# Optimization experiments

Measured on AMD Instinct MI355X. Metric: run time of the kernel, lower is better.

The kernel has to match this reference:

```python
import jax, jax.numpy as jnp
import numpy as np

T = 20000          # document length in tokens
EMBED_DIM = 300    # GloVe 840B.300d
STATE_DIM = 400    # 2 * lstm_dim (bidirectional)
HIDDEN = 150       # Scorer hidden_dim default
MAX_N = 10         # span widths 1..10
G_DIM = 2 * STATE_DIM + EMBED_DIM  # 1100


def _mlp3(x, W1, b1, W2, b2, W3, b3):
    # Scorer: Linear -> ReLU -> Linear -> ReLU -> Linear(->1)
    h = jax.nn.relu(x @ W1 + b1)
    h = jax.nn.relu(h @ W2 + b2)
    return h @ W3 + b3


def _span_features(embeds, states, attn_logits):
    """Vectorized SpanEncoder: for every window of width n in 1..MAX_N,
    softmax the per-token attention logits within the window, attention-pool
    the word embeddings, and concat [state_start, state_end, pooled].
    Returns g of shape [sum_n (T-n+1), G_DIM]."""
    gs = []
    for n in range(1, MAX_N + 1):
        S = T - n + 1  # number of width-n spans
        # [n, S] windowed logits and [n, S, E] windowed embeds via shifted slices
        a = jnp.stack([attn_logits[j:j + S] for j in range(n)], axis=0)
        w = jax.nn.softmax(a, axis=0)  # softmax within each span (dim=0 in torch)
        we = jnp.stack([embeds[j:j + S] for j in range(n)], axis=0)
        pooled = jnp.einsum('ns,nse->se', w, we)  # [S, E]
        g = jnp.concatenate([states[:S], states[n - 1:n - 1 + S], pooled], axis=-1)
        gs.append(g)
    return jnp.concatenate(gs, axis=0)


def setup_inputs() -> dict:
    key = jax.random.key(0)
    ks = jax.random.split(key, 16)
    sc = 0.05
    return {
        'embeds': jax.random.normal(ks[0], (T, EMBED_DIM), jnp.float32),
        'states': jax.random.normal(ks[1], (T, STATE_DIM), jnp.float32),
        'attn_W1': jax.random.normal(ks[2], (STATE_DIM, HIDDEN), jnp.float32) * sc,
        'attn_b1': jnp.zeros((HIDDEN,), jnp.float32),
        'attn_W2': jax.random.normal(ks[3], (HIDDEN, HIDDEN), jnp.float32) * sc,
        'attn_b2': jnp.zeros((HIDDEN,), jnp.float32),
        'attn_W3': jax.random.normal(ks[4], (HIDDEN, 1), jnp.float32) * sc,
        'attn_b3': jnp.zeros((1,), jnp.float32),
        'sc_W1': jax.random.normal(ks[5], (G_DIM, HIDDEN), jnp.float32) * sc,
        'sc_b1': jnp.zeros((HIDDEN,), jnp.float32),
        'sc_W2': jax.random.normal(ks[6], (HIDDEN, HIDDEN), jnp.float32) * sc,
        'sc_b2': jnp.zeros((HIDDEN,), jnp.float32),
        'sc_W3': jax.random.normal(ks[7], (HIDDEN, 1), jnp.float32) * sc,
        'sc_b3': jnp.zeros((1,), jnp.float32),
    }


def reference(embeds, states, attn_W1, attn_b1, attn_W2, attn_b2, attn_W3, attn_b3,
              sc_W1, sc_b1, sc_W2, sc_b2, sc_W3, sc_b3):
    # SpanAttention: per-token scalar attention logit from the BiLSTM state
    attn_logits = _mlp3(states, attn_W1, attn_b1, attn_W2, attn_b2, attn_W3, attn_b3)[:, 0]
    # SpanEncoder: ragged windowed attention pooling + boundary-state concat
    g = _span_features(embeds, states, attn_logits)  # [10T-45, 1100]
    # SpanScorer: MLP score per span
    scores = _mlp3(g, sc_W1, sc_b1, sc_W2, sc_b2, sc_W3, sc_b3)[:, 0]
    return scores
```

## Files before the change

kernel.cpp:

```cpp
#include <hip/hip_runtime.h>
#include <hip/hip_bf16.h>
#include <math.h>

#define T_LEN 20000
#define HID 150
#define STR 168

typedef __attribute__((ext_vector_type(8))) __bf16 bf16x8;
typedef __attribute__((ext_vector_type(4))) float f32x4;

__device__ __forceinline__ short f2bf(float f) {
    unsigned u = __float_as_uint(f);
    u = (u + 0x7fff + ((u >> 16) & 1)) >> 16;
    return (short)u;
}

__device__ __forceinline__ unsigned pk2(float a, float b) {
    __hip_bfloat162 h = __float22bfloat162_rn(make_float2(a, b));
    return *(unsigned*)&h;
}

__device__ __forceinline__ bf16x8 cvt8(float4 a, float4 b) {
    union { unsigned u[4]; bf16x8 v; } r;
    r.u[0] = pk2(a.x, a.y);
    r.u[1] = pk2(a.z, a.w);
    r.u[2] = pk2(b.x, b.y);
    r.u[3] = pk2(b.z, b.w);
    return r.v;
}

__device__ __forceinline__ float2 ubf2(unsigned u) {
    return make_float2(__uint_as_float(u << 16),
                       __uint_as_float(u & 0xffff0000u));
}

__global__ __launch_bounds__(256) void wprep(
    const float* __restrict__ sc_W1, const float* __restrict__ attn_W1,
    const float* __restrict__ attn_W2, const float* __restrict__ sc_W2,
    short* __restrict__ frag)
{
    int t = blockIdx.x * 256 + threadIdx.x;
    if (t >= 302080) return;
    float v = 0.f;
    if (t < 199680) {
        int e = t & 7, g = t >> 3;
        int lane = g & 63, h = g >> 6;
        int ks = h % 13, nt = h / 13;
        int k = ks * 32 + (lane >> 4) * 8 + e;
        int cs = (nt % 10) * 16 + (lane & 15);
        if (k < 400 && cs < HID) {
            if (nt < 10)      v = sc_W1[(long)k * HID + cs];
            else if (nt < 20) v = sc_W1[(long)(400 + k) * HID + cs];
            else              v = attn_W1[(long)k * HID + cs];
        }
    } else if (t < 250880) {
        int r = t - 199680;
        int e = r & 7, g = r >> 3;
        int lane = g & 63, h = g >> 6;
        int ks = h % 10, nt = h / 10;
        int k = ks * 32 + (lane >> 4) * 8 + e;
        int cs = nt * 16 + (lane & 15);
        if (k < 300 && cs < HID) v = sc_W1[(long)(800 + k) * HID + cs];
    } else if (t < 276480) {
        int r = t - 250880;
        int e = r & 7, g = r >> 3;
        int lane = g & 63, h = g >> 6;
        int ks = h % 5, nt = h / 5;
        int k = ks * 32 + (lane >> 4) * 8 + e;
        int cs = nt * 16 + (lane & 15);
        if (k < HID && cs < HID) v = attn_W2[(long)k * HID + cs];
    } else {
        int r = t - 276480;
        int e = r & 7, g = r >> 3;
        int lane = g & 63, h = g >> 6;
        int ks = h % 5, nt = h / 5;
        int k = ks * 32 + (lane >> 4) * 8 + e;
        int cs = nt * 16 + (lane & 15);
        if (k < HID && cs < HID) v = sc_W2[(long)k * HID + cs];
    }
    frag[t] = f2bf(v);
}

__global__ __launch_bounds__(384) void mega(
    const float* __restrict__ states, const float* __restrict__ embeds,
    const short* __restrict__ frag,
    const float* __restrict__ scb1, const float* __restrict__ ab1,
    const float* __restrict__ ab2, const float* __restrict__ aW3,
    const float* __restrict__ ab3,
    const float* __restrict__ b2, const float* __restrict__ W3,
    const float* __restrict__ b3,
    float* __restrict__ out)
{
    __shared__ short AsU[19968];
    __shared__ short Us[32 * STR];
    __shared__ short Vs[48 * STR];
    __shared__ short Ps[48 * STR];
    __shared__ short X1s[48 * STR];
    __shared__ float redl[48][6];
    __shared__ float reds[2][32][2];
    __shared__ float Ls[48], ebuf[48];
    __shared__ float sb1[160], ab1s[160], b2s[160], W3s[160];

    const int tid = threadIdx.x;
    const int w = tid >> 6, lane = tid & 63;
    const int ml = lane & 15, kg = lane >> 4;
    const int s0 = blockIdx.x * 32;

    for (int t = tid; t < 160; t += 384) {
        sb1[t]  = (t < HID) ? scb1[t] : 0.f;
        ab1s[t] = (t < HID) ? ab1[t]  : 0.f;
        b2s[t]  = (t < HID) ? b2[t]   : 0.f;
        W3s[t]  = (t < HID) ? W3[t]   : 0.f;
    }

    for (int idx = tid; idx < 2496; idx += 384) {
        int g = idx / 832, r = idx - g * 832;
        int ks = r >> 6, l2 = r & 63;
        int k = ks * 32 + ((l2 >> 4) << 3);
        int row = s0 + g * 16 + (l2 & 15); if (row > T_LEN - 1) row = T_LEN - 1;
        const float* Ar = states + (long)row * 400;
        float4 a0 = make_float4(0.f, 0.f, 0.f, 0.f), a1 = a0;
        if (k + 4 <= 400) a0 = *(const float4*)&Ar[k];
        if (k + 8 <= 400) a1 = *(const float4*)&Ar[k + 4];
        *(bf16x8*)&AsU[idx * 8] = cvt8(a0, a1);
    }
    __syncthreads();

    {
        f32x4 acc[5][3];
        #pragma unroll
        for (int t = 0; t < 5; ++t)
            #pragma unroll
            for (int g = 0; g < 3; ++g)
                acc[t][g] = (f32x4){0.f, 0.f, 0.f, 0.f};

        const short* fb = frag + lane * 8;
        const int t5 = w * 5;
        bf16x8 bcur[5], bnxt[5];
        #pragma unroll
        for (int t = 0; t < 5; ++t)
            bcur[t] = *(const bf16x8*)&fb[((t5 + t) * 13) << 9];

        #pragma unroll
        for (int ks = 0; ks < 13; ++ks) {
            if (ks < 12) {
                #pragma unroll
                for (int t = 0; t < 5; ++t)
                    bnxt[t] = *(const bf16x8*)&fb[((t5 + t) * 13 + ks + 1) << 9];
            }
            bf16x8 af0 = *(const bf16x8*)&AsU[(ks * 64 + lane) * 8];
            bf16x8 af1 = *(const bf16x8*)&AsU[(832 + ks * 64 + lane) * 8];
            bf16x8 af2_ = *(const bf16x8*)&AsU[(1664 + ks * 64 + lane) * 8];
            #pragma unroll
            for (int t = 0; t < 5; ++t) {
                acc[t][0] = __builtin_amdgcn_mfma_f32_16x16x32_bf16(bcur[t], af0, acc[t][0], 0, 0, 0);
                acc[t][1] = __builtin_amdgcn_mfma_f32_16x16x32_bf16(bcur[t], af1, acc[t][1], 0, 0, 0);
                acc[t][2] = __builtin_amdgcn_mfma_f32_16x16x32_bf16(bcur[t], af2_, acc[t][2], 0, 0, 0);
            }
            #pragma unroll
            for (int t = 0; t < 5; ++t) bcur[t] = bnxt[t];
        }

        #pragma unroll
        for (int t = 0; t < 5; ++t) {
            int nt = t5 + t;
            #pragma unroll
            for (int g = 0; g < 3; ++g) {
                if (w < 2) {
                    if (g < 2) {
                        int col0 = nt * 16 + kg * 4;
                        float v[4];
                        #pragma unroll
                        for (int r = 0; r < 4; ++r) {
                            int c = col0 + r;
                            v[r] = (c < HID) ? acc[t][g][r] + sb1[c] : 0.f;
                        }
                        *(uint2*)&Us[(g * 16 + ml) * STR + col0] =
                            make_uint2(pk2(v[0], v[1]), pk2(v[2], v[3]));
                    }
                } else if (w < 4) {
                    int col0 = (nt - 10) * 16 + kg * 4;
                    float v[4];
                    #pragma unroll
                    for (int r = 0; r < 4; ++r) {
                        int c = col0 + r;
                        v[r] = (c < HID) ? acc[t][g][r] : 0.f;
                    }
                    *(uint2*)&Vs[(g * 16 + ml) * STR + col0] =
                        make_uint2(pk2(v[0], v[1]), pk2(v[2], v[3]));
                } else {
                    int col0 = (nt - 20) * 16 + kg * 4;
                    float v[4];
                    #pragma unroll
                    for (int r = 0; r < 4; ++r) {
                        int c = col0 + r;
                        v[r] = (c < HID) ? fmaxf(acc[t][g][r] + ab1s[c], 0.f) : 0.f;
                    }
                    *(uint2*)&X1s[(g * 16 + ml) * STR + col0] =
                        make_uint2(pk2(v[0], v[1]), pk2(v[2], v[3]));
                }
            }
        }
    }
    __syncthreads();

    for (int idx = tid; idx < 1920; idx += 384) {
        int g = idx / 640, r = idx - g * 640;
        int ks = r >> 6, l2 = r & 63;
        int k = ks * 32 + ((l2 >> 4) << 3);
        int row = s0 + g * 16 + (l2 & 15); if (row > T_LEN - 1) row = T_LEN - 1;
        const float* Er = embeds + (long)row * 300;
        float4 a0 = make_float4(0.f, 0.f, 0.f, 0.f), a1 = a0;
        if (k + 4 <= 300) a0 = *(const float4*)&Er[k];
        if (k + 8 <= 300) a1 = *(const float4*)&Er[k + 4];
        *(bf16x8*)&AsU[idx * 8] = cvt8(a0, a1);
    }
    __syncthreads();

    const int tB = (w < 4) ? 2 * w : (w == 4 ? 8 : 9);
    const int nTP = (w < 4) ? 2 : 1;
    {
        f32x4 accP[2][3];
        #pragma unroll
        for (int t = 0; t < 2; ++t)
            #pragma unroll
            for (int g = 0; g < 3; ++g)
                accP[t][g] = (f32x4){0.f, 0.f, 0.f, 0.f};

        const short* fP = frag + 199680 + lane * 8;
        bf16x8 pcur[2], pnxt[2];
        #pragma unroll
        for (int t = 0; t < 2; ++t)
            if (t < nTP) pcur[t] = *(const bf16x8*)&fP[((tB + t) * 10) << 9];

        #pragma unroll
        for (int ks = 0; ks < 10; ++ks) {
            if (ks < 9) {
                #pragma unroll
                for (int t = 0; t < 2; ++t)
                    if (t < nTP) pnxt[t] = *(const bf16x8*)&fP[((tB + t) * 10 + ks + 1) << 9];
            }
            bf16x8 af0 = *(const bf16x8*)&AsU[(ks * 64 + lane) * 8];
            bf16x8 af1 = *(const bf16x8*)&AsU[(640 + ks * 64 + lane) * 8];
            bf16x8 af2_ = *(const bf16x8*)&AsU[(1280 + ks * 64 + lane) * 8];
            #pragma unroll
            for (int t = 0; t < 2; ++t) {
                if (t < nTP) {
                    accP[t][0] = __builtin_amdgcn_mfma_f32_16x16x32_bf16(pcur[t], af0, accP[t][0], 0, 0, 0);
                    accP[t][1] = __builtin_amdgcn_mfma_f32_16x16x32_bf16(pcur[t], af1, accP[t][1], 0, 0, 0);
                    accP[t][2] = __builtin_amdgcn_mfma_f32_16x16x32_bf16(pcur[t], af2_, accP[t][2], 0, 0, 0);
                }
            }
            #pragma unroll
            for (int t = 0; t < 2; ++t) pcur[t] = pnxt[t];
        }

        #pragma unroll
        for (int t = 0; t < 2; ++t) {
            if (t < nTP) {
                int col0 = (tB + t) * 16 + kg * 4;
                #pragma unroll
                for (int g = 0; g < 3; ++g) {
                    float v[4];
                    #pragma unroll
                    for (int r = 0; r < 4; ++r) {
                        int c = col0 + r;
                        v[r] = (c < HID) ? accP[t][g][r] : 0.f;
                    }
                    *(uint2*)&Ps[(g * 16 + ml) * STR + col0] =
                        make_uint2(pk2(v[0], v[1]), pk2(v[2], v[3]));
                }
            }
        }
    }

    {
        const short* fAt2 = frag + 250880 + lane * 8;
        bf16x8 afx[3][5];
        #pragma unroll
        for (int g = 0; g < 3; ++g)
            #pragma unroll
            for (int ks = 0; ks < 5; ++ks)
                afx[g][ks] = *(const bf16x8*)&X1s[(g * 16 + ml) * STR + ks * 32 + kg * 8];

        float score[3][4];
        #pragma unroll
        for (int g = 0; g < 3; ++g)
            #pragma unroll
            for (int r = 0; r < 4; ++r) score[g][r] = 0.f;

        #pragma unroll
        for (int t = 0; t < 2; ++t) {
            if (t < nTP) {
                int nt = tB + t;
                bf16x8 wb[5];
                #pragma unroll
                for (int ks = 0; ks < 5; ++ks)
                    wb[ks] = *(const bf16x8*)&fAt2[(nt * 5 + ks) << 9];
                f32x4 a2[3];
                a2[0] = (f32x4){0.f, 0.f, 0.f, 0.f};
                a2[1] = (f32x4){0.f, 0.f, 0.f, 0.f};
                a2[2] = (f32x4){0.f, 0.f, 0.f, 0.f};
                #pragma unroll
                for (int g = 0; g < 3; ++g)
                    #pragma unroll
                    for (int ks = 0; ks < 5; ++ks)
                        a2[g] = __builtin_amdgcn_mfma_f32_16x16x32_bf16(afx[g][ks], wb[ks], a2[g], 0, 0, 0);
                int col = nt * 16 + ml;
                float b2v = (col < HID) ? ab2[col] : 0.f;
                float w3v = (col < HID) ? aW3[col] : 0.f;
                #pragma unroll
                for (int g = 0; g < 3; ++g)
                    #pragma unroll
                    for (int r = 0; r < 4; ++r)
                        score[g][r] += fmaxf(a2[g][r] + b2v, 0.f) * w3v;
            }
        }
        #pragma unroll
        for (int g = 0; g < 3; ++g)
            #pragma unroll
            for (int r = 0; r < 4; ++r) {
                score[g][r] += __shfl_xor(score[g][r], 1);
                score[g][r] += __shfl_xor(score[g][r], 2);
                score[g][r] += __shfl_xor(score[g][r], 4);
                score[g][r] += __shfl_xor(score[g][r], 8);
            }
        if (ml == 0) {
            #pragma unroll
            for (int g = 0; g < 3; ++g)
                #pragma unroll
                for (int r = 0; r < 4; ++r)
                    redl[g * 16 + kg * 4 + r][w] = score[g][r];
        }
    }
    __syncthreads();

    if (tid < 48) {
        float Lv = redl[tid][0] + redl[tid][1] + redl[tid][2] +
                   redl[tid][3] + redl[tid][4] + redl[tid][5] + ab3[0];
        Ls[tid] = (tid < 41) ? Lv : -1e30f;
    }
    if (tid < 48) {
        float M = -1e30f;
        for (int t = 0; t < 41; ++t) M = fmaxf(M, Ls[t]);
        ebuf[tid] = (tid < 41) ? expf(Ls[tid] - M) : 0.f;
    }

    float Ur[2][20], accp[2][20], den[2];
    const int u = tid & 127;
    if (w >= 4) {
        #pragma unroll
        for (int z = 0; z < 2; ++z) {
            int uz = u + z * 128;
            int iz = uz >> 3, d0z = 20 * (uz & 7);
            const uint2* U2 = (const uint2*)&Us[iz * STR + d0z];
            #pragma unroll
            for (int c = 0; c < 5; ++c) {
                uint2 uv = U2[c];
                float2 a = ubf2(uv.x), b_ = ubf2(uv.y);
                Ur[z][4 * c + 0] = a.x;  Ur[z][4 * c + 1] = a.y;
                Ur[z][4 * c + 2] = b_.x; Ur[z][4 * c + 3] = b_.y;
            }
            #pragma unroll
            for (int d = 0; d < 20; ++d) accp[z][d] = 0.f;
            den[z] = 0.f;
        }
    }
    __syncthreads();

    short* h1p = AsU;

    auto phase1 = [&](int n, int p) {
        #pragma unroll
        for (int z = 0; z < 2; ++z) {
            int uz = u + z * 128;
            int iz = uz >> 3, d0z = 20 * (uz & 7);
            int l = iz + n - 1;
            float e = ebuf[l];
            den[z] += e;
            const uint2* P2 = (const uint2*)&Ps[l * STR + d0z];
            #pragma unroll
            for (int c = 0; c < 5; ++c) {
                uint2 pv = P2[c];
                float2 a = ubf2(pv.x), b_ = ubf2(pv.y);
                accp[z][4 * c + 0] += e * a.x;  accp[z][4 * c + 1] += e * a.y;
                accp[z][4 * c + 2] += e * b_.x; accp[z][4 * c + 3] += e * b_.y;
            }
            float invd = 1.f / den[z];
            const uint2* V2 = (const uint2*)&Vs[l * STR + d0z];
            #pragma unroll
            for (int c = 0; c < 5; ++c) {
                uint2 vv = V2[c];
                float2 a = ubf2(vv.x), b_ = ubf2(vv.y);
                float x0 = fmaxf(Ur[z][4 * c + 0] + a.x  + accp[z][4 * c + 0] * invd, 0.f);
                float x1 = fmaxf(Ur[z][4 * c + 1] + a.y  + accp[z][4 * c + 1] * invd, 0.f);
                float x2 = fmaxf(Ur[z][4 * c + 2] + b_.x + accp[z][4 * c + 2] * invd, 0.f);
                float x3 = fmaxf(Ur[z][4 * c + 3] + b_.y + accp[z][4 * c + 3] * invd, 0.f);
                *(uint2*)&h1p[p * (32 * STR) + iz * STR + d0z + 4 * c] =
                    make_uint2(pk2(x0, x1), pk2(x2, x3));
            }
        }
    };

    if (w >= 4) phase1(1, 0);
    __syncthreads();

    const int mt = w >> 1;
    const int nt0 = (w & 1) * 5;
    const short* fW2 = frag + 276480;
    const float bb = b3[0];

    for (int n = 1; n <= 10; ++n) {
        const int p = (n - 1) & 1;
        if (w >= 4) {
            if (n < 10) phase1(n + 1, 1 - p);
        } else {
            bf16x8 af[5];
            #pragma unroll
            for (int ks = 0; ks < 5; ++ks)
                af[ks] = *(const bf16x8*)&h1p[p * (32 * STR) + (mt * 16 + ml) * STR + ks * 32 + kg * 8];

            float sc[4] = {0.f, 0.f, 0.f, 0.f};
            #pragma unroll
            for (int j = 0; j < 5; ++j) {
                int nt = nt0 + j;
                f32x4 a2 = {0.f, 0.f, 0.f, 0.f};
                #pragma unroll
                for (int ks = 0; ks < 5; ++ks) {
                    bf16x8 bf = *(const bf16x8*)&fW2[(long)(((nt * 5 + ks) << 6) | lane) << 3];
                    a2 = __builtin_amdgcn_mfma_f32_16x16x32_bf16(af[ks], bf, a2, 0, 0, 0);
                }
                int col = nt * 16 + ml;
                float b2v = b2s[col], w3v = W3s[col];
                #pragma unroll
                for (int r = 0; r < 4; ++r)
                    sc[r] += fmaxf(a2[r] + b2v, 0.f) * w3v;
            }
            #pragma unroll
            for (int r = 0; r < 4; ++r) {
                sc[r] += __shfl_xor(sc[r], 1);
                sc[r] += __shfl_xor(sc[r], 2);
                sc[r] += __shfl_xor(sc[r], 4);
                sc[r] += __shfl_xor(sc[r], 8);
            }
            if (ml == 0) {
                #pragma unroll
                for (int r = 0; r < 4; ++r)
                    reds[p][mt * 16 + kg * 4 + r][w & 1] = sc[r];
            }
        }
        __syncthreads();
        if (tid < 32) {
            int S = T_LEN - n + 1;
            int off = (n - 1) * (T_LEN + 1) - (n - 1) * n / 2;
            int sr = s0 + tid;
            if (sr < S) out[off + sr] = reds[p][tid][0] + reds[p][tid][1] + bb;
        }
    }
}

extern "C" void kernel_launch(void* const* d_in, const int* in_sizes, int n_in,
                              void* d_out, int out_size, void* d_ws, size_t ws_size,
                              hipStream_t stream) {
    const float* embeds  = (const float*)d_in[0];
    const float* states  = (const float*)d_in[1];
    const float* attn_W1 = (const float*)d_in[2];
    const float* attn_b1 = (const float*)d_in[3];
    const float* attn_W2 = (const float*)d_in[4];
    const float* attn_b2 = (const float*)d_in[5];
    const float* attn_W3 = (const float*)d_in[6];
    const float* attn_b3 = (const float*)d_in[7];
    const float* sc_W1   = (const float*)d_in[8];
    const float* sc_b1   = (const float*)d_in[9];
    const float* sc_W2   = (const float*)d_in[10];
    const float* sc_b2   = (const float*)d_in[11];
    const float* sc_W3   = (const float*)d_in[12];
    const float* sc_b3   = (const float*)d_in[13];
    float* out = (float*)d_out;

    short* frag = (short*)d_ws;

    wprep<<<1180, 256, 0, stream>>>(sc_W1, attn_W1, attn_W2, sc_W2, frag);
    mega<<<625, 384, 0, stream>>>(states, embeds, frag, sc_b1, attn_b1,
                                  attn_b2, attn_W3, attn_b3,
                                  sc_b2, sc_W3, sc_b3, out);
}
```

Measured before the change: 230.2 us.

## Raise mega kernel to 512 threads with K-chunked staging and reduced LDS

The fused kernel moves from 6 to 8 waves per block and loads the states and embeds tiles in two K-chunks through a smaller shared staging buffer. The attention-MLP second layer now runs before the embeds projection, so its input buffer can be reused for the projected embeds, and the phase-1 pooling work is spread so each thread handles one span slot instead of two. The aim is lower LDS use and register pressure for more resident waves and better latency hiding. The cost is extra barriers per chunk and a changed LDS stride that may affect bank conflicts.

```diff
diff --git a/kernel.cpp b/kernel.cpp
--- a/kernel.cpp
+++ b/kernel.cpp
@@ -4,7 +4,8 @@
 
 #define T_LEN 20000
 #define HID 150
-#define STR 168
+#define STRU 168
+#define STRPV 176
 
 typedef __attribute__((ext_vector_type(8))) __bf16 bf16x8;
 typedef __attribute__((ext_vector_type(4))) float f32x4;
@@ -81,7 +82,56 @@
     frag[t] = f2bf(v);
 }
 
-__global__ __launch_bounds__(384) void mega(
+template<int KC>
+__device__ __forceinline__ void stage48(const float* __restrict__ src, int K,
+                                        int ks0, int s0, int tid, short* RA)
+{
+    for (int idx = tid; idx < 3 * KC * 64; idx += 512) {
+        int g = idx / (KC * 64), r = idx - g * (KC * 64);
+        int ksl = r >> 6, l2 = r & 63;
+        int k = (ks0 + ksl) * 32 + ((l2 >> 4) << 3);
+        int row = s0 + g * 16 + (l2 & 15); if (row > T_LEN - 1) row = T_LEN - 1;
+        const float* Ar = src + (long)row * K;
+        float4 a0 = make_float4(0.f, 0.f, 0.f, 0.f), a1 = a0;
+        if (k + 4 <= K) a0 = *(const float4*)&Ar[k];
+        if (k + 8 <= K) a1 = *(const float4*)&Ar[k + 4];
+        *(bf16x8*)&RA[idx * 8] = cvt8(a0, a1);
+    }
+}
+
+template<int KC, int NT>
+__device__ __forceinline__ void mm48(const short* __restrict__ fb, const short* RA,
+                                     int lane, int ks0, int t0, int kstot,
+                                     f32x4 (*acc)[3])
+{
+    bf16x8 bcur[NT], bnxt[NT];
+    #pragma unroll
+    for (int t = 0; t < NT; ++t)
+        bcur[t] = *(const bf16x8*)&fb[((t0 + t) * kstot + ks0) << 9];
+    #pragma unroll
+    for (int ksl = 0; ksl < KC; ++ksl) {
+        if (ksl < KC - 1) {
+            #pragma unroll
+            for (int t = 0; t < NT; ++t)
+                bnxt[t] = *(const bf16x8*)&fb[((t0 + t) * kstot + ks0 + ksl + 1) << 9];
+        }
+        bf16x8 af0 = *(const bf16x8*)&RA[((0 * KC + ksl) * 64 + lane) * 8];
+        bf16x8 af1 = *(const bf16x8*)&RA[((1 * KC + ksl) * 64 + lane) * 8];
+        bf16x8 af2 = *(const bf16x8*)&RA[((2 * KC + ksl) * 64 + lane) * 8];
+        #pragma unroll
+        for (int t = 0; t < NT; ++t) {
+            acc[t][0] = __builtin_amdgcn_mfma_f32_16x16x32_bf16(bcur[t], af0, acc[t][0], 0, 0, 0);
+            acc[t][1] = __builtin_amdgcn_mfma_f32_16x16x32_bf16(bcur[t], af1, acc[t][1], 0, 0, 0);
+            acc[t][2] = __builtin_amdgcn_mfma_f32_16x16x32_bf16(bcur[t], af2, acc[t][2], 0, 0, 0);
+        }
+        if (ksl < KC - 1) {
+            #pragma unroll
+            for (int t = 0; t < NT; ++t) bcur[t] = bnxt[t];
+        }
+    }
+}
+
+__global__ __launch_bounds__(512, 4) void mega(
     const float* __restrict__ states, const float* __restrict__ embeds,
     const short* __restrict__ frag,
     const float* __restrict__ scb1, const float* __restrict__ ab1,
@@ -91,12 +141,11 @@
     const float* __restrict__ b3,
     float* __restrict__ out)
 {
-    __shared__ short AsU[19968];
-    __shared__ short Us[32 * STR];
-    __shared__ short Vs[48 * STR];
-    __shared__ short Ps[48 * STR];
-    __shared__ short X1s[48 * STR];
-    __shared__ float redl[48][6];
+    __shared__ short RA[10752];
+    __shared__ short XPs[48 * STRPV];
+    __shared__ short Us[32 * STRU];
+    __shared__ short Vs[48 * STRPV];
+    __shared__ float redl[48][8];
     __shared__ float reds[2][32][2];
     __shared__ float Ls[48], ebuf[48];
     __shared__ float sb1[160], ab1s[160], b2s[160], W3s[160];
@@ -106,119 +155,152 @@
     const int ml = lane & 15, kg = lane >> 4;
     const int s0 = blockIdx.x * 32;
 
-    for (int t = tid; t < 160; t += 384) {
+    for (int t = tid; t < 160; t += 512) {
         sb1[t]  = (t < HID) ? scb1[t] : 0.f;
         ab1s[t] = (t < HID) ? ab1[t]  : 0.f;
         b2s[t]  = (t < HID) ? b2[t]   : 0.f;
         W3s[t]  = (t < HID) ? W3[t]   : 0.f;
     }
 
-    for (int idx = tid; idx < 2496; idx += 384) {
-        int g = idx / 832, r = idx - g * 832;
-        int ks = r >> 6, l2 = r & 63;
-        int k = ks * 32 + ((l2 >> 4) << 3);
-        int row = s0 + g * 16 + (l2 & 15); if (row > T_LEN - 1) row = T_LEN - 1;
-        const float* Ar = states + (long)row * 400;
-        float4 a0 = make_float4(0.f, 0.f, 0.f, 0.f), a1 = a0;
-        if (k + 4 <= 400) a0 = *(const float4*)&Ar[k];
-        if (k + 8 <= 400) a1 = *(const float4*)&Ar[k + 4];
-        *(bf16x8*)&AsU[idx * 8] = cvt8(a0, a1);
-    }
-    __syncthreads();
-
+    const short* fb = frag + lane * 8;
+
+    const int nTA = (w < 6) ? 4 : 3;
+    const int t0A = (w < 6) ? 4 * w : 24 + (w - 6) * 3;
     {
-        f32x4 acc[5][3];
-        #pragma unroll
-        for (int t = 0; t < 5; ++t)
+        f32x4 acc[4][3];
+        #pragma unroll
+        for (int t = 0; t < 4; ++t)
             #pragma unroll
             for (int g = 0; g < 3; ++g)
                 acc[t][g] = (f32x4){0.f, 0.f, 0.f, 0.f};
 
-        const short* fb = frag + lane * 8;
-        const int t5 = w * 5;
-        bf16x8 bcur[5], bnxt[5];
-        #pragma unroll
-        for (int t = 0; t < 5; ++t)
-            bcur[t] = *(const bf16x8*)&fb[((t5 + t) * 13) << 9];
-
-        #pragma unroll
-        for (int ks = 0; ks < 13; ++ks) {
-            if (ks < 12) {
-                #pragma unroll
-                for (int t = 0; t < 5; ++t)
-                    bnxt[t] = *(const bf16x8*)&fb[((t5 + t) * 13 + ks + 1) << 9];
-            }
-            bf16x8 af0 = *(const bf16x8*)&AsU[(ks * 64 + lane) * 8];
-            bf16x8 af1 = *(const bf16x8*)&AsU[(832 + ks * 64 + lane) * 8];
-            bf16x8 af2_ = *(const bf16x8*)&AsU[(1664 + ks * 64 + lane) * 8];
-            #pragma unroll
-            for (int t = 0; t < 5; ++t) {
-                acc[t][0] = __builtin_amdgcn_mfma_f32_16x16x32_bf16(bcur[t], af0, acc[t][0], 0, 0, 0);
-                acc[t][1] = __builtin_amdgcn_mfma_f32_16x16x32_bf16(bcur[t], af1, acc[t][1], 0, 0, 0);
-                acc[t][2] = __builtin_amdgcn_mfma_f32_16x16x32_bf16(bcur[t], af2_, acc[t][2], 0, 0, 0);
-            }
-            #pragma unroll
-            for (int t = 0; t < 5; ++t) bcur[t] = bnxt[t];
-        }
-
-        #pragma unroll
-        for (int t = 0; t < 5; ++t) {
-            int nt = t5 + t;
-            #pragma unroll
-            for (int g = 0; g < 3; ++g) {
-                if (w < 2) {
-                    if (g < 2) {
-                        int col0 = nt * 16 + kg * 4;
+        stage48<7>(states, 400, 0, s0, tid, RA);
+        __syncthreads();
+        if (w < 6) mm48<7, 4>(fb, RA, lane, 0, t0A, 13, acc);
+        else       mm48<7, 3>(fb, RA, lane, 0, t0A, 13, acc);
+        __syncthreads();
+        stage48<6>(states, 400, 7, s0, tid, RA);
+        __syncthreads();
+        if (w < 6) mm48<6, 4>(fb, RA, lane, 7, t0A, 13, acc);
+        else       mm48<6, 3>(fb, RA, lane, 7, t0A, 13, acc);
+
+        #pragma unroll
+        for (int t = 0; t < 4; ++t) {
+            if (t < nTA) {
+                int nt = t0A + t;
+                #pragma unroll
+                for (int g = 0; g < 3; ++g) {
+                    if (nt < 10) {
+                        if (g < 2) {
+                            int col0 = nt * 16 + kg * 4;
+                            float v[4];
+                            #pragma unroll
+                            for (int r = 0; r < 4; ++r) {
+                                int c = col0 + r;
+                                v[r] = (c < HID) ? acc[t][g][r] + sb1[c] : 0.f;
+                            }
+                            *(uint2*)&Us[(g * 16 + ml) * STRU + col0] =
+                                make_uint2(pk2(v[0], v[1]), pk2(v[2], v[3]));
+                        }
+                    } else if (nt < 20) {
+                        int col0 = (nt - 10) * 16 + kg * 4;
                         float v[4];
                         #pragma unroll
                         for (int r = 0; r < 4; ++r) {
                             int c = col0 + r;
-                            v[r] = (c < HID) ? acc[t][g][r] + sb1[c] : 0.f;
+                            v[r] = (c < HID) ? acc[t][g][r] : 0.f;
                         }
-                        *(uint2*)&Us[(g * 16 + ml) * STR + col0] =
+                        *(uint2*)&Vs[(g * 16 + ml) * STRPV + col0] =
+                            make_uint2(pk2(v[0], v[1]), pk2(v[2], v[3]));
+                    } else {
+                        int col0 = (nt - 20) * 16 + kg * 4;
+                        float v[4];
+                        #pragma unroll
+                        for (int r = 0; r < 4; ++r) {
+                            int c = col0 + r;
+                            v[r] = (c < HID) ? fmaxf(acc[t][g][r] + ab1s[c], 0.f) : 0.f;
+                        }
+                        *(uint2*)&XPs[(g * 16 + ml) * STRU + col0] =
                             make_uint2(pk2(v[0], v[1]), pk2(v[2], v[3]));
                     }
-                } else if (w < 4) {
-                    int col0 = (nt - 10) * 16 + kg * 4;
-                    float v[4];
+                }
+            }
+        }
+    }
+    __syncthreads();
+
+    const int nTP = (w < 2) ? 2 : 1;
+    const int tB = (w < 2) ? 2 * w : 2 + w;
+    {
+        const short* fAt2 = frag + 250880 + lane * 8;
+        bf16x8 afx[3][5];
+        #pragma unroll
+        for (int g = 0; g < 3; ++g)
+            #pragma unroll
+            for (int ks = 0; ks < 5; ++ks)
+                afx[g][ks] = *(const bf16x8*)&XPs[(g * 16 + ml) * STRU + ks * 32 + kg * 8];
+
+        float score[3][4];
+        #pragma unroll
+        for (int g = 0; g < 3; ++g)
+            #pragma unroll
+            for (int r = 0; r < 4; ++r) score[g][r] = 0.f;
+
+        #pragma unroll
+        for (int t = 0; t < 2; ++t) {
+            if (t < nTP) {
+                int nt = tB + t;
+                bf16x8 wb[5];
+                #pragma unroll
+                for (int ks = 0; ks < 5; ++ks)
+                    wb[ks] = *(const bf16x8*)&fAt2[(nt * 5 + ks) << 9];
+                f32x4 a2[3];
+                a2[0] = (f32x4){0.f, 0.f, 0.f, 0.f};
+                a2[1] = (f32x4){0.f, 0.f, 0.f, 0.f};
+                a2[2] = (f32x4){0.f, 0.f, 0.f, 0.f};
+                #pragma unroll
+                for (int g = 0; g < 3; ++g)
                     #pragma unroll
-                    for (int r = 0; r < 4; ++r) {
-                        int c = col0 + r;
-                        v[r] = (c < HID) ? acc[t][g][r] : 0.f;
-                    }
-                    *(uint2*)&Vs[(g * 16 + ml) * STR + col0] =
-                        make_uint2(pk2(v[0], v[1]), pk2(v[2], v[3]));
-                } else {
-                    int col0 = (nt - 20) * 16 + kg * 4;
-                    float v[4];
+                    for (int ks = 0; ks < 5; ++ks)
+                        a2[g] = __builtin_amdgcn_mfma_f32_16x16x32_bf16(afx[g][ks], wb[ks], a2[g], 0, 0, 0);
+                int col = nt * 16 + ml;
+                float b2v = (col < HID) ? ab2[col] : 0.f;
+                float w3v = (col < HID) ? aW3[col] : 0.f;
+                #pragma unroll
+                for (int g = 0; g < 3; ++g)
                     #pragma unroll
-                    for (int r = 0; r < 4; ++r) {
-                        int c = col0 + r;
-                        v[r] = (c < HID) ? fmaxf(acc[t][g][r] + ab1s[c], 0.f) : 0.f;
-                    }
-                    *(uint2*)&X1s[(g * 16 + ml) * STR + col0] =
-                        make_uint2(pk2(v[0], v[1]), pk2(v[2], v[3]));
-                }
-            }
+                    for (int r = 0; r < 4; ++r)
+                        score[g][r] += fmaxf(a2[g][r] + b2v, 0.f) * w3v;
+            }
+        }
+        #pragma unroll
+        for (int g = 0; g < 3; ++g)
+            #pragma unroll
+            for (int r = 0; r < 4; ++r) {
+                score[g][r] += __shfl_xor(score[g][r], 1);
+                score[g][r] += __shfl_xor(score[g][r], 2);
+                score[g][r] += __shfl_xor(score[g][r], 4);
+                score[g][r] += __shfl_xor(score[g][r], 8);
+            }
+        if (ml == 0) {
+            #pragma unroll
+            for (int g = 0; g < 3; ++g)
+                #pragma unroll
+                for (int r = 0; r < 4; ++r)
+                    redl[g * 16 + kg * 4 + r][w] = score[g][r];
         }
     }
     __syncthreads();
 
-    for (int idx = tid; idx < 1920; idx += 384) {
-        int g = idx / 640, r = idx - g * 640;
-        int ks = r >> 6, l2 = r & 63;
-        int k = ks * 32 + ((l2 >> 4) << 3);
-        int row = s0 + g * 16 + (l2 & 15); if (row > T_LEN - 1) row = T_LEN - 1;
-        const float* Er = embeds + (long)row * 300;
-        float4 a0 = make_float4(0.f, 0.f, 0.f, 0.f), a1 = a0;
-        if (k + 4 <= 300) a0 = *(const float4*)&Er[k];
-        if (k + 8 <= 300) a1 = *(const float4*)&Er[k + 4];
-        *(bf16x8*)&AsU[idx * 8] = cvt8(a0, a1);
-    }
-    __syncthreads();
-
-    const int tB = (w < 4) ? 2 * w : (w == 4 ? 8 : 9);
-    const int nTP = (w < 4) ? 2 : 1;
+    if (tid < 48) {
+        float Lv = redl[tid][0] + redl[tid][1] + redl[tid][2] + redl[tid][3] +
+                   redl[tid][4] + redl[tid][5] + redl[tid][6] + redl[tid][7] + ab3[0];
+        Ls[tid] = (tid < 41) ? Lv : -1e30f;
+        float M = -1e30f;
+        for (int t = 0; t < 41; ++t) M = fmaxf(M, Ls[t]);
+        ebuf[tid] = (tid < 41) ? expf(Ls[tid] - M) : 0.f;
+    }
+
     {
         f32x4 accP[2][3];
         #pragma unroll
@@ -228,32 +310,15 @@
                 accP[t][g] = (f32x4){0.f, 0.f, 0.f, 0.f};
 
         const short* fP = frag + 199680 + lane * 8;
-        bf16x8 pcur[2], pnxt[2];
-        #pragma unroll
-        for (int t = 0; t < 2; ++t)
-            if (t < nTP) pcur[t] = *(const bf16x8*)&fP[((tB + t) * 10) << 9];
-
-        #pragma unroll
-        for (int ks = 0; ks < 10; ++ks) {
-            if (ks < 9) {
-                #pragma unroll
-                for (int t = 0; t < 2; ++t)
-                    if (t < nTP) pnxt[t] = *(const bf16x8*)&fP[((tB + t) * 10 + ks + 1) << 9];
-            }
-            bf16x8 af0 = *(const bf16x8*)&AsU[(ks * 64 + lane) * 8];
-            bf16x8 af1 = *(const bf16x8*)&AsU[(640 + ks * 64 + lane) * 8];
-            bf16x8 af2_ = *(const bf16x8*)&AsU[(1280 + ks * 64 + lane) * 8];
-            #pragma unroll
-            for (int t = 0; t < 2; ++t) {
-                if (t < nTP) {
-                    accP[t][0] = __builtin_amdgcn_mfma_f32_16x16x32_bf16(pcur[t], af0, accP[t][0], 0, 0, 0);
-                    accP[t][1] = __builtin_amdgcn_mfma_f32_16x16x32_bf16(pcur[t], af1, accP[t][1], 0, 0, 0);
-                    accP[t][2] = __builtin_amdgcn_mfma_f32_16x16x32_bf16(pcur[t], af2_, accP[t][2], 0, 0, 0);
-                }
-            }
-            #pragma unroll
-            for (int t = 0; t < 2; ++t) pcur[t] = pnxt[t];
-        }
+        stage48<5>(embeds, 300, 0, s0, tid, RA);
+        __syncthreads();
+        if (w < 2) mm48<5, 2>(fP, RA, lane, 0, tB, 10, accP);
+        else       mm48<5, 1>(fP, RA, lane, 0, tB, 10, accP);
+        __syncthreads();
+        stage48<5>(embeds, 300, 5, s0, tid, RA);
+        __syncthreads();
+        if (w < 2) mm48<5, 2>(fP, RA, lane, 5, tB, 10, accP);
+        else       mm48<5, 1>(fP, RA, lane, 5, tB, 10, accP);
 
         #pragma unroll
         for (int t = 0; t < 2; ++t) {
@@ -267,138 +332,56 @@
                         int c = col0 + r;
                         v[r] = (c < HID) ? accP[t][g][r] : 0.f;
                     }
-                    *(uint2*)&Ps[(g * 16 + ml) * STR + col0] =
+                    *(uint2*)&XPs[(g * 16 + ml) * STRPV + col0] =
                         make_uint2(pk2(v[0], v[1]), pk2(v[2], v[3]));
                 }
             }
         }
     }
 
-    {
-        const short* fAt2 = frag + 250880 + lane * 8;
-        bf16x8 afx[3][5];
-        #pragma unroll
-        for (int g = 0; g < 3; ++g)
-            #pragma unroll
-            for (int ks = 0; ks < 5; ++ks)
-                afx[g][ks] = *(const bf16x8*)&X1s[(g * 16 + ml) * STR + ks * 32 + kg * 8];
-
-        float score[3][4];
-        #pragma unroll
-        for (int g = 0; g < 3; ++g)
-            #pragma unroll
-            for (int r = 0; r < 4; ++r) score[g][r] = 0.f;
-
-        #pragma unroll
-        for (int t = 0; t < 2; ++t) {
-            if (t < nTP) {
-                int nt = tB + t;
-                bf16x8 wb[5];
-                #pragma unroll
-                for (int ks = 0; ks < 5; ++ks)
-                    wb[ks] = *(const bf16x8*)&fAt2[(nt * 5 + ks) << 9];
-                f32x4 a2[3];
-                a2[0] = (f32x4){0.f, 0.f, 0.f, 0.f};
-                a2[1] = (f32x4){0.f, 0.f, 0.f, 0.f};
-                a2[2] = (f32x4){0.f, 0.f, 0.f, 0.f};
-                #pragma unroll
-                for (int g = 0; g < 3; ++g)
-                    #pragma unroll
-                    for (int ks = 0; ks < 5; ++ks)
-                        a2[g] = __builtin_amdgcn_mfma_f32_16x16x32_bf16(afx[g][ks], wb[ks], a2[g], 0, 0, 0);
-                int col = nt * 16 + ml;
-                float b2v = (col < HID) ? ab2[col] : 0.f;
-                float w3v = (col < HID) ? aW3[col] : 0.f;
-                #pragma unroll
-                for (int g = 0; g < 3; ++g)
-                    #pragma unroll
-                    for (int r = 0; r < 4; ++r)
-                        score[g][r] += fmaxf(a2[g][r] + b2v, 0.f) * w3v;
-            }
-        }
-        #pragma unroll
-        for (int g = 0; g < 3; ++g)
-            #pragma unroll
-            for (int r = 0; r < 4; ++r) {
-                score[g][r] += __shfl_xor(score[g][r], 1);
-                score[g][r] += __shfl_xor(score[g][r], 2);
-                score[g][r] += __shfl_xor(score[g][r], 4);
-                score[g][r] += __shfl_xor(score[g][r], 8);
-            }
-        if (ml == 0) {
-            #pragma unroll
-            for (int g = 0; g < 3; ++g)
-                #pragma unroll
-                for (int r = 0; r < 4; ++r)
-                    redl[g * 16 + kg * 4 + r][w] = score[g][r];
-        }
+    float Ur[20], accp[20], den = 0.f;
+    const int u2 = tid - 256;
+    const int iz = u2 >> 3, q = u2 & 7, d0 = 20 * (u2 & 7);
+    if (w >= 4) {
+        const uint2* U2 = (const uint2*)&Us[iz * STRU + d0];
+        #pragma unroll
+        for (int c = 0; c < 5; ++c) {
+            uint2 uv = U2[c];
+            float2 a = ubf2(uv.x), b_ = ubf2(uv.y);
+            Ur[4 * c + 0] = a.x;  Ur[4 * c + 1] = a.y;
+            Ur[4 * c + 2] = b_.x; Ur[4 * c + 3] = b_.y;
+        }
+        #pragma unroll
+        for (int d = 0; d < 20; ++d) accp[d] = 0.f;
     }
     __syncthreads();
 
-    if (tid < 48) {
-        float Lv = redl[tid][0] + redl[tid][1] + redl[tid][2] +
-                   redl[tid][3] + redl[tid][4] + redl[tid][5] + ab3[0];
-        Ls[tid] = (tid < 41) ? Lv : -1e30f;
-    }
-    if (tid < 48) {
-        float M = -1e30f;
-        for (int t = 0; t < 41; ++t) M = fmaxf(M, Ls[t]);
-        ebuf[tid] = (tid < 41) ? expf(Ls[tid] - M) : 0.f;
-    }
-
-    float Ur[2][20], accp[2][20], den[2];
-    const int u = tid & 127;
-    if (w >= 4) {
-        #pragma unroll
-        for (int z = 0; z < 2; ++z) {
-            int uz = u + z * 128;
-            int iz = uz >> 3, d0z = 20 * (uz & 7);
-            const uint2* U2 = (const uint2*)&Us[iz * STR + d0z];
-            #pragma unroll
-            for (int c = 0; c < 5; ++c) {
-                uint2 uv = U2[c];
-                float2 a = ubf2(uv.x), b_ = ubf2(uv.y);
-                Ur[z][4 * c + 0] = a.x;  Ur[z][4 * c + 1] = a.y;
-                Ur[z][4 * c + 2] = b_.x; Ur[z][4 * c + 3] = b_.y;
-            }
-            #pragma unroll
-            for (int d = 0; d < 20; ++d) accp[z][d] = 0.f;
-            den[z] = 0.f;
-        }
-    }
-    __syncthreads();
-
-    short* h1p = AsU;
+    short* h1p = RA;
 
     auto phase1 = [&](int n, int p) {
-        #pragma unroll
-        for (int z = 0; z < 2; ++z) {
-            int uz = u + z * 128;
-            int iz = uz >> 3, d0z = 20 * (uz & 7);
-            int l = iz + n - 1;
-            float e = ebuf[l];
-            den[z] += e;
-            const uint2* P2 = (const uint2*)&Ps[l * STR + d0z];
-            #pragma unroll
-            for (int c = 0; c < 5; ++c) {
-                uint2 pv = P2[c];
-                float2 a = ubf2(pv.x), b_ = ubf2(pv.y);
-                accp[z][4 * c + 0] += e * a.x;  accp[z][4 * c + 1] += e * a.y;
-                accp[z][4 * c + 2] += e * b_.x; accp[z][4 * c + 3] += e * b_.y;
-            }
-            float invd = 1.f / den[z];
-            const uint2* V2 = (const uint2*)&Vs[l * STR + d0z];
-            #pragma unroll
-            for (int c = 0; c < 5; ++c) {
-                uint2 vv = V2[c];
-                float2 a = ubf2(vv.x), b_ = ubf2(vv.y);
-                float x0 = fmaxf(Ur[z][4 * c + 0] + a.x  + accp[z][4 * c + 0] * invd, 0.f);
-                float x1 = fmaxf(Ur[z][4 * c + 1] + a.y  + accp[z][4 * c + 1] * invd, 0.f);
-                float x2 = fmaxf(Ur[z][4 * c + 2] + b_.x + accp[z][4 * c + 2] * invd, 0.f);
-                float x3 = fmaxf(Ur[z][4 * c + 3] + b_.y + accp[z][4 * c + 3] * invd, 0.f);
-                *(uint2*)&h1p[p * (32 * STR) + iz * STR + d0z + 4 * c] =
-                    make_uint2(pk2(x0, x1), pk2(x2, x3));
-            }
+        int l = iz + n - 1;
+        float e = ebuf[l];
+        den += e;
+        const uint2* P2 = (const uint2*)&XPs[l * STRPV + d0];
+        #pragma unroll
+        for (int c = 0; c < 5; ++c) {
+            uint2 pv = P2[c];
+            float2 a = ubf2(pv.x), b_ = ubf2(pv.y);
+            accp[4 * c + 0] += e * a.x;  accp[4 * c + 1] += e * a.y;
+            accp[4 * c + 2] += e * b_.x; accp[4 * c + 3] += e * b_.y;
+        }
+        float invd = 1.f / den;
+        const uint2* V2 = (const uint2*)&Vs[l * STRPV + d0];
+        #pragma unroll
+        for (int c = 0; c < 5; ++c) {
+            uint2 vv = V2[c];
+            float2 a = ubf2(vv.x), b_ = ubf2(vv.y);
+            float x0 = fmaxf(Ur[4 * c + 0] + a.x  + accp[4 * c + 0] * invd, 0.f);
+            float x1 = fmaxf(Ur[4 * c + 1] + a.y  + accp[4 * c + 1] * invd, 0.f);
+            float x2 = fmaxf(Ur[4 * c + 2] + b_.x + accp[4 * c + 2] * invd, 0.f);
+            float x3 = fmaxf(Ur[4 * c + 3] + b_.y + accp[4 * c + 3] * invd, 0.f);
+            *(uint2*)&h1p[p * (32 * STRU) + iz * STRU + d0 + 4 * c] =
+                make_uint2(pk2(x0, x1), pk2(x2, x3));
         }
     };
 
@@ -418,7 +401,7 @@
             bf16x8 af[5];
             #pragma unroll
             for (int ks = 0; ks < 5; ++ks)
-                af[ks] = *(const bf16x8*)&h1p[p * (32 * STR) + (mt * 16 + ml) * STR + ks * 32 + kg * 8];
+                af[ks] = *(const bf16x8*)&h1p[p * (32 * STRU) + (mt * 16 + ml) * STRU + ks * 32 + kg * 8];
 
             float sc[4] = {0.f, 0.f, 0.f, 0.f};
             #pragma unroll
@@ -481,7 +464,7 @@
     short* frag = (short*)d_ws;
 
     wprep<<<1180, 256, 0, stream>>>(sc_W1, attn_W1, attn_W2, sc_W2, frag);
-    mega<<<625, 384, 0, stream>>>(states, embeds, frag, sc_b1, attn_b1,
+    mega<<<625, 512, 0, stream>>>(states, embeds, frag, sc_b1, attn_b1,
                                   attn_b2, attn_W3, attn_b3,
                                   sc_b2, sc_W3, sc_b3, out);
 }
```

Result: slower. 244.2 us (+6.1%).
